# Optimization experiments

Measured on AMD Instinct MI355X. Metric: run time of the kernel, lower is better.

The kernel has to match this reference:

```python
import jax, jax.numpy as jnp
import numpy as np

C = 128
NUM_HEADS = 8
KEY_DIM = C // NUM_HEADS  # 16
BN_EPS = 1e-5


def setup_inputs() -> dict:
    key = jax.random.key(0)
    ks = jax.random.split(key, 6)
    B, H, W = 8, 32, 32
    stddev = KEY_DIM ** (-0.5)
    return {
        "x": jax.random.normal(ks[0], (B, C, H, W), dtype=jnp.float32),
        "gamma": jnp.ones((C,), dtype=jnp.float32),
        "beta": jnp.zeros((C,), dtype=jnp.float32),
        "wq": jax.random.normal(ks[1], (C, C), dtype=jnp.float32) * 0.05,
        "wk": jax.random.normal(ks[2], (C, C), dtype=jnp.float32) * 0.05,
        "wv": jax.random.normal(ks[3], (C, C), dtype=jnp.float32) * 0.05,
        "pos_emb_h": jax.random.uniform(ks[4], (2 * H - 1,), dtype=jnp.float32) * stddev,
        "pos_emb_w": jax.random.uniform(ks[5], (2 * W - 1,), dtype=jnp.float32) * stddev,
    }


def _rel_bias(pos_emb, L):
    # torch: pos_emb.unfold(0, L, 1).flip(-1) -> emb[i, k] = pos_emb[i + (L-1) - k]
    idx = jnp.arange(L)[:, None] + (L - 1) - jnp.arange(L)[None, :]
    return pos_emb[idx]  # [L, L]


def reference(x, gamma, beta, wq, wk, wv, pos_emb_h, pos_emb_w):
    B, _, H, W = x.shape
    N = H * W
    qk_scale = 1.0 / np.sqrt(np.float32(KEY_DIM))

    # BatchNorm2d (training-mode batch stats, biased variance) + exact GELU
    mean = jnp.mean(x, axis=(0, 2, 3), keepdims=True)
    var = jnp.var(x, axis=(0, 2, 3), keepdims=True)
    out = (x - mean) * jax.lax.rsqrt(var + BN_EPS)
    out = out * gamma[None, :, None, None] + beta[None, :, None, None]
    out = jax.nn.gelu(out, approximate=False)

    # 1x1 convs == per-pixel linear maps, then split heads and flatten spatial
    def proj(w):
        y = jnp.einsum('oc,bchw->bohw', w, out)
        return y.reshape(B, NUM_HEADS, KEY_DIM, N)  # [B, h, d, N]

    q = proj(wq) * qk_scale
    k = proj(wk)
    v = proj(wv)

    scores = jnp.einsum('bhdq,bhdk->bhqk', q, k)  # [B, h, N, N]

    h_emb = _rel_bias(pos_emb_h, H)  # [H, H]
    w_emb = _rel_bias(pos_emb_w, W)  # [W, W]
    emb = (h_emb[:, None, :, None] + w_emb[None, :, None, :]).reshape(N, N)
    scores = scores + emb[None, None, :, :]

    attn = jax.nn.softmax(scores, axis=-1)
    o = jnp.einsum('bhqk,bhdk->bhdq', attn, v)  # [B, h, d, N]
    o = o.reshape(B, C, H, W)
    return x + o
```

## Files before the change

### kernel.cpp

```cpp
#include <hip/hip_runtime.h>
#include <hip/hip_bf16.h>
#include <math.h>

typedef short bf4 __attribute__((ext_vector_type(4)));
typedef float f32x4 __attribute__((ext_vector_type(4)));

constexpr int CC  = 128;
constexpr int NH  = 8;
constexpr int KD  = 16;
constexpr int BB  = 8;
constexpr int NN  = 1024;
constexpr int BHW = BB * NN;
constexpr float LOG2E = 1.44269504088896340736f;
constexpr float MBOUND = 32.0f;

static __device__ __forceinline__ short f2bf(float x) {
    __hip_bfloat16 b = __float2bfloat16(x);
    short s;
    __builtin_memcpy(&s, &b, 2);
    return s;
}
static __device__ __forceinline__ unsigned fbits(float x) {
    unsigned u;
    __builtin_memcpy(&u, &x, 4);
    return u;
}
static __device__ __forceinline__ float fexp2(float x) {
#if __has_builtin(__builtin_amdgcn_exp2f)
    return __builtin_amdgcn_exp2f(x);
#else
    return exp2f(x);
#endif
}

static __device__ __forceinline__ f32x4 mfma16(bf4 a, bf4 b, f32x4 c) {
#if __has_builtin(__builtin_amdgcn_mfma_f32_16x16x16bf16_1k)
    return __builtin_amdgcn_mfma_f32_16x16x16bf16_1k(a, b, c, 0, 0, 0);
#else
    f32x4 d;
    asm volatile("v_mfma_f32_16x16x16_bf16 %0, %1, %2, %3"
                 : "=&v"(d) : "v"(a), "v"(b), "v"(c));
    return d;
#endif
}

__global__ __launch_bounds__(256) void k_prep(const float* __restrict__ x,
                                              const float* __restrict__ wq,
                                              const float* __restrict__ wk,
                                              const float* __restrict__ wv,
                                              float* __restrict__ ps,
                                              short* __restrict__ wf) {
    int t = threadIdx.x;
    int blk = blockIdx.x;
    if (blk < 256) {
        int c = blk >> 1, half = blk & 1;
        float s1 = 0.f, s2 = 0.f;
        #pragma unroll
        for (int k = 0; k < 4; ++k) {
            int b = half * 4 + k;
            float4 v = ((const float4*)(x + ((size_t)b * CC + c) * NN))[t];
            s1 += v.x + v.y + v.z + v.w;
            s2 += v.x * v.x + v.y * v.y + v.z * v.z + v.w * v.w;
        }
        #pragma unroll
        for (int off = 32; off >= 1; off >>= 1) {
            s1 += __shfl_xor(s1, off);
            s2 += __shfl_xor(s2, off);
        }
        __shared__ float r1[4], r2[4];
        int wid = t >> 6, lane = t & 63;
        if (lane == 0) { r1[wid] = s1; r2[wid] = s2; }
        __syncthreads();
        if (t == 0) {
            ps[c * 4 + half * 2 + 0] = r1[0] + r1[1] + r1[2] + r1[3];
            ps[c * 4 + half * 2 + 1] = r2[0] + r2[1] + r2[2] + r2[3];
        }
    } else {
        int s = (blk - 256) * 256 + t;
        int ln = s & 63, ct = (s >> 6) & 7, mt = (s >> 9) & 7, p = s >> 12;
        int hl = ln >> 4, li = ln & 15;
        const float* w = (p == 0) ? wq : (p == 1) ? wk : wv;
        float4 v = *(const float4*)(w + (size_t)(mt * 16 + li) * CC + ct * 16 + 4 * hl);
        float sc = (p == 0) ? 0.25f * LOG2E : 1.0f;
        bf4 r;
        r[0] = f2bf(v.x * sc); r[1] = f2bf(v.y * sc);
        r[2] = f2bf(v.z * sc); r[3] = f2bf(v.w * sc);
        *(bf4*)&wf[(size_t)s * 4] = r;
    }
}

__global__ __launch_bounds__(512) void k_proj(const float* __restrict__ x,
                                              const float* __restrict__ ps,
                                              const float* __restrict__ gamma,
                                              const float* __restrict__ beta,
                                              const short* __restrict__ wf,
                                              short* __restrict__ qf,
                                              short* __restrict__ kf,
                                              short* __restrict__ vf) {
    __shared__ float xS[128][20];
    __shared__ float ssS[256];
    __shared__ short afS[8][256];
    int it = blockIdx.x, b = blockIdx.y;
    int t = threadIdx.x;
    if (t < 128) {
        int c = t;
        float4 p4 = *(const float4*)(ps + c * 4);
        float s1 = p4.x + p4.z;
        float s2 = p4.y + p4.w;
        float mean = s1 / (float)BHW;
        float var  = s2 / (float)BHW - mean * mean;
        float rstd = rsqrtf(var + 1e-5f);
        float sc = rstd * gamma[c];
        ssS[c]       = sc;
        ssS[128 + c] = beta[c] - mean * sc;
    }
    const float* xb = x + (size_t)b * CC * NN + it * 16;
    {
        int r = t >> 2, cf = t & 3;
        float4 v = *(const float4*)(xb + (size_t)r * NN + cf * 4);
        *(float4*)&xS[r][cf * 4] = v;
    }
    __syncthreads();
    {
        int ct = t >> 6, ln = t & 63;
        int hl_ = ln >> 4, li_ = ln & 15;
        int c0 = ct * 16 + 4 * hl_;
        bf4 r;
        #pragma unroll
        for (int jj = 0; jj < 4; ++jj) {
            int c = c0 + jj;
            float v = xS[c][li_] * ssS[c] + ssS[128 + c];
            v = 0.5f * v * (1.0f + erff(v * 0.70710678f));
            r[jj] = f2bf(v);
        }
        *(bf4*)&afS[ct][ln * 4] = r;
    }
    __syncthreads();

    int wid = t >> 6, lane = t & 63;
    int hl = lane >> 4, li = lane & 15;
    f32x4 acc[3];
    #pragma unroll
    for (int e = 0; e < 3; ++e) acc[e] = (f32x4)0.f;
    #pragma unroll
    for (int ct = 0; ct < 8; ++ct) {
        bf4 af = *(const bf4*)&afS[ct][lane * 4];
        #pragma unroll
        for (int e = 0; e < 3; ++e) {
            int mtp = wid + 8 * e;
            bf4 wfr = *(const bf4*)(wf + ((size_t)(mtp * 8 + ct) * 64 + lane) * 4);
            acc[e] = mfma16(wfr, af, acc[e]);
        }
    }
    int bq = b * 8;
    #pragma unroll
    for (int e = 0; e < 2; ++e) {
        short* dst = (e == 0) ? qf : kf;
        bf4 r;
        #pragma unroll
        for (int jr = 0; jr < 4; ++jr) r[jr] = f2bf(acc[e][jr]);
        *(bf4*)&dst[(((size_t)(bq + wid) * 64 + it) * 64 + lane) * 4] = r;
    }
    {
        float* vScrW = &xS[0][0] + wid * 272;
        #pragma unroll
        for (int r = 0; r < 4; ++r)
            vScrW[(4 * hl + r) * 17 + li] = acc[2][r];
        bf4 r;
        #pragma unroll
        for (int jj = 0; jj < 4; ++jj)
            r[jj] = f2bf(vScrW[li * 17 + 4 * hl + jj]);
        *(bf4*)&vf[(((size_t)(bq + wid) * 64 + it) * 64 + lane) * 4] = r;
    }
}

__global__ __launch_bounds__(512) void k_attn(const short* __restrict__ qf,
                                              const short* __restrict__ kf,
                                              const short* __restrict__ vf,
                                              const float* __restrict__ x,
                                              const float* __restrict__ peh,
                                              const float* __restrict__ pew,
                                              float* __restrict__ out) {
    __shared__ short ldsK[16384];
    __shared__ short ldsV[16384];
    __shared__ float phS[64], pwS[64];
    int t = threadIdx.x;
    int bh = blockIdx.x;
    const short* qfh = qf + (size_t)bh * 16384;
    const short* kfh = kf + (size_t)bh * 16384;
    const short* vfh = vf + (size_t)bh * 16384;

    #pragma unroll
    for (int k = 0; k < 4; ++k)
        ((int4*)ldsK)[t + 512 * k] = ((const int4*)kfh)[t + 512 * k];
    #pragma unroll
    for (int k = 0; k < 4; ++k)
        ((int4*)ldsV)[t + 512 * k] = ((const int4*)vfh)[t + 512 * k];
    if (t < 64) {
        phS[t] = (t < 63) ? peh[t] * LOG2E : -1e30f;
        pwS[t] = (t < 63) ? pew[t] * LOG2E : -1e30f;
    }
    __syncthreads();

    int wid = t >> 6, lane = t & 63;
    int li = lane & 15, hl = lane >> 4;
    int it = blockIdx.y * 8 + wid;

    bf4 qfr = *(const bf4*)(qfh + ((size_t)it * 64 + lane) * 4);

    int wi = ((it & 1) << 4) | li;
    float pwm[2][4];
    #pragma unroll
    for (int jp = 0; jp < 2; ++jp)
        #pragma unroll
        for (int r = 0; r < 4; ++r)
            pwm[jp][r] = pwS[wi + 31 - ((jp << 4) + 4 * hl + r)] - MBOUND;

    int hq = it >> 1;
    const float* phBase = &phS[hq];
    const short* kBase = &ldsK[lane * 4];
    const short* vBase = &ldsV[lane * 4];

    f32x4 oaccA = (f32x4)0.f, oaccB = (f32x4)0.f;
    f32x4 lacc0 = (f32x4)0.f, lacc1 = (f32x4)0.f;
    short oneb = (short)0x3F80;
    bf4 ones = {oneb, oneb, oneb, oneb};

    #pragma unroll
    for (int ch = 0; ch < 16; ++ch) {
        float ph0 = phBase[31 - 2 * ch];
        float ph1 = phBase[30 - 2 * ch];
        bf4 kb[4], vb[4];
        #pragma unroll
        for (int jt = 0; jt < 4; ++jt) {
            kb[jt] = *(const bf4*)(kBase + (ch * 4 + jt) * 256);
            vb[jt] = *(const bf4*)(vBase + (ch * 4 + jt) * 256);
        }
        f32x4 s[4];
        #pragma unroll
        for (int jt = 0; jt < 4; ++jt) {
            float ph = (jt < 2) ? ph0 : ph1;
            f32x4 c;
            #pragma unroll
            for (int r = 0; r < 4; ++r) c[r] = pwm[jt & 1][r] + ph;
            s[jt] = mfma16(kb[jt], qfr, c);
        }
        #pragma unroll
        for (int jt = 0; jt < 4; ++jt)
            #pragma unroll
            for (int r = 0; r < 4; ++r)
                s[jt][r] = fexp2(s[jt][r]);
        bf4 pf[4];
        #pragma unroll
        for (int jt = 0; jt < 4; ++jt) {
            unsigned lo = __builtin_amdgcn_perm(fbits(s[jt][1]), fbits(s[jt][0]), 0x07060302u);
            unsigned hi = __builtin_amdgcn_perm(fbits(s[jt][3]), fbits(s[jt][2]), 0x07060302u);
            unsigned pk[2] = {lo, hi};
            __builtin_memcpy(&pf[jt], pk, 8);
        }
        oaccA = mfma16(vb[0], pf[0], oaccA);
        oaccB = mfma16(vb[2], pf[2], oaccB);
        lacc0 = mfma16(ones,  pf[0], lacc0);
        lacc1 = mfma16(ones,  pf[2], lacc1);
        oaccA = mfma16(vb[1], pf[1], oaccA);
        oaccB = mfma16(vb[3], pf[3], oaccB);
        lacc0 = mfma16(ones,  pf[1], lacc0);
        lacc1 = mfma16(ones,  pf[3], lacc1);
    }

    float rl = 1.0f / (lacc0[0] + lacc1[0]);

    int b = bh >> 3, h = bh & 7;
    size_t base = (size_t)b * (CC * NN) + (size_t)h * KD * NN;
    int i = it * 16 + li;
    #pragma unroll
    for (int r = 0; r < 4; ++r) {
        int d = 4 * hl + r;
        size_t g = base + (size_t)d * NN + i;
        out[g] = x[g] + (oaccA[r] + oaccB[r]) * rl;
    }
}

extern "C" void kernel_launch(void* const* d_in, const int* in_sizes, int n_in,
                              void* d_out, int out_size, void* d_ws, size_t ws_size,
                              hipStream_t stream) {
    const float* x     = (const float*)d_in[0];
    const float* gamma = (const float*)d_in[1];
    const float* beta  = (const float*)d_in[2];
    const float* wq    = (const float*)d_in[3];
    const float* wk    = (const float*)d_in[4];
    const float* wv    = (const float*)d_in[5];
    const float* peh   = (const float*)d_in[6];
    const float* pew   = (const float*)d_in[7];
    float* out = (float*)d_out;
    float* ws  = (float*)d_ws;

    float* ps = ws;
    short* wf = (short*)(ws + 512);
    short* qf = wf + 49152;
    short* kf = qf + (1 << 20);
    short* vf = kf + (1 << 20);

    k_prep<<<304, 256, 0, stream>>>(x, wq, wk, wv, ps, wf);
    k_proj<<<dim3(64, 8), 512, 0, stream>>>(x, ps, gamma, beta, wf, qf, kf, vf);
    k_attn<<<dim3(64, 8), 512, 0, stream>>>(qf, kf, vf, x, peh, pew, out);
}
```

Before: 33.16 us.

## Split BN stats into per-(channel,batch) blocks and software-pipeline QK MFMA in attention

```diff
diff --git a/kernel.cpp b/kernel.cpp
--- a/kernel.cpp
+++ b/kernel.cpp
@@ -52,16 +52,11 @@
                                               short* __restrict__ wf) {
     int t = threadIdx.x;
     int blk = blockIdx.x;
-    if (blk < 256) {
-        int c = blk >> 1, half = blk & 1;
-        float s1 = 0.f, s2 = 0.f;
-        #pragma unroll
-        for (int k = 0; k < 4; ++k) {
-            int b = half * 4 + k;
-            float4 v = ((const float4*)(x + ((size_t)b * CC + c) * NN))[t];
-            s1 += v.x + v.y + v.z + v.w;
-            s2 += v.x * v.x + v.y * v.y + v.z * v.z + v.w * v.w;
-        }
+    if (blk < 1024) {
+        int c = blk >> 3, b = blk & 7;
+        float4 v = ((const float4*)(x + ((size_t)b * CC + c) * NN))[t];
+        float s1 = v.x + v.y + v.z + v.w;
+        float s2 = v.x * v.x + v.y * v.y + v.z * v.z + v.w * v.w;
         #pragma unroll
         for (int off = 32; off >= 1; off >>= 1) {
             s1 += __shfl_xor(s1, off);
@@ -72,11 +67,11 @@
         if (lane == 0) { r1[wid] = s1; r2[wid] = s2; }
         __syncthreads();
         if (t == 0) {
-            ps[c * 4 + half * 2 + 0] = r1[0] + r1[1] + r1[2] + r1[3];
-            ps[c * 4 + half * 2 + 1] = r2[0] + r2[1] + r2[2] + r2[3];
+            ps[(c * 8 + b) * 2 + 0] = r1[0] + r1[1] + r1[2] + r1[3];
+            ps[(c * 8 + b) * 2 + 1] = r2[0] + r2[1] + r2[2] + r2[3];
         }
     } else {
-        int s = (blk - 256) * 256 + t;
+        int s = (blk - 1024) * 256 + t;
         int ln = s & 63, ct = (s >> 6) & 7, mt = (s >> 9) & 7, p = s >> 12;
         int hl = ln >> 4, li = ln & 15;
         const float* w = (p == 0) ? wq : (p == 1) ? wk : wv;
@@ -104,9 +99,10 @@
     int t = threadIdx.x;
     if (t < 128) {
         int c = t;
-        float4 p4 = *(const float4*)(ps + c * 4);
-        float s1 = p4.x + p4.z;
-        float s2 = p4.y + p4.w;
+        const float4* pp = (const float4*)(ps + c * 16);
+        float4 a0 = pp[0], a1 = pp[1], a2 = pp[2], a3 = pp[3];
+        float s1 = a0.x + a0.z + a1.x + a1.z + a2.x + a2.z + a3.x + a3.z;
+        float s2 = a0.y + a0.w + a1.y + a1.w + a2.y + a2.w + a3.y + a3.w;
         float mean = s1 / (float)BHW;
         float var  = s2 / (float)BHW - mean * mean;
         float rstd = rsqrtf(var + 1e-5f);
@@ -226,35 +222,40 @@
     short oneb = (short)0x3F80;
     bf4 ones = {oneb, oneb, oneb, oneb};
 
-    #pragma unroll
-    for (int ch = 0; ch < 16; ++ch) {
+    auto qk = [&](int ch, f32x4* s) {
         float ph0 = phBase[31 - 2 * ch];
         float ph1 = phBase[30 - 2 * ch];
-        bf4 kb[4], vb[4];
         #pragma unroll
         for (int jt = 0; jt < 4; ++jt) {
-            kb[jt] = *(const bf4*)(kBase + (ch * 4 + jt) * 256);
-            vb[jt] = *(const bf4*)(vBase + (ch * 4 + jt) * 256);
-        }
-        f32x4 s[4];
-        #pragma unroll
-        for (int jt = 0; jt < 4; ++jt) {
+            bf4 kb = *(const bf4*)(kBase + (ch * 4 + jt) * 256);
             float ph = (jt < 2) ? ph0 : ph1;
             f32x4 c;
             #pragma unroll
             for (int r = 0; r < 4; ++r) c[r] = pwm[jt & 1][r] + ph;
-            s[jt] = mfma16(kb[jt], qfr, c);
-        }
+            s[jt] = mfma16(kb, qfr, c);
+        }
+    };
+
+    f32x4 s_cur[4];
+    qk(0, s_cur);
+    #pragma unroll
+    for (int ch = 0; ch < 16; ++ch) {
+        f32x4 s_nxt[4];
+        if (ch < 15) qk(ch + 1, s_nxt);
+        bf4 vb[4];
+        #pragma unroll
+        for (int jt = 0; jt < 4; ++jt)
+            vb[jt] = *(const bf4*)(vBase + (ch * 4 + jt) * 256);
         #pragma unroll
         for (int jt = 0; jt < 4; ++jt)
             #pragma unroll
             for (int r = 0; r < 4; ++r)
-                s[jt][r] = fexp2(s[jt][r]);
+                s_cur[jt][r] = fexp2(s_cur[jt][r]);
         bf4 pf[4];
         #pragma unroll
         for (int jt = 0; jt < 4; ++jt) {
-            unsigned lo = __builtin_amdgcn_perm(fbits(s[jt][1]), fbits(s[jt][0]), 0x07060302u);
-            unsigned hi = __builtin_amdgcn_perm(fbits(s[jt][3]), fbits(s[jt][2]), 0x07060302u);
+            unsigned lo = __builtin_amdgcn_perm(fbits(s_cur[jt][1]), fbits(s_cur[jt][0]), 0x07060302u);
+            unsigned hi = __builtin_amdgcn_perm(fbits(s_cur[jt][3]), fbits(s_cur[jt][2]), 0x07060302u);
             unsigned pk[2] = {lo, hi};
             __builtin_memcpy(&pf[jt], pk, 8);
         }
@@ -266,6 +267,8 @@
         oaccB = mfma16(vb[3], pf[3], oaccB);
         lacc0 = mfma16(ones,  pf[1], lacc0);
         lacc1 = mfma16(ones,  pf[3], lacc1);
+        #pragma unroll
+        for (int jt = 0; jt < 4; ++jt) s_cur[jt] = s_nxt[jt];
     }
 
     float rl = 1.0f / (lacc0[0] + lacc1[0]);
@@ -296,12 +299,12 @@
     float* ws  = (float*)d_ws;
 
     float* ps = ws;
-    short* wf = (short*)(ws + 512);
+    short* wf = (short*)(ws + 2048);
     short* qf = wf + 49152;
     short* kf = qf + (1 << 20);
     short* vf = kf + (1 << 20);
 
-    k_prep<<<304, 256, 0, stream>>>(x, wq, wk, wv, ps, wf);
+    k_prep<<<1072, 256, 0, stream>>>(x, wq, wk, wv, ps, wf);
     k_proj<<<dim3(64, 8), 512, 0, stream>>>(x, ps, gamma, beta, wf, qf, kf, vf);
     k_attn<<<dim3(64, 8), 512, 0, stream>>>(qf, kf, vf, x, peh, pew, out);
 }
```

Result: no change. 32.72 us (-1.3%).
